# Kernel optimization log

Hardware: AMD Instinct MI355X
Metric: run time of the kernel (lower is better)

## Reference

```python
import jax, jax.numpy as jnp
import numpy as np
import math

HIDDEN = 1024
N_HEADS = 16
HEAD_DIM = HIDDEN // N_HEADS

def _safe(x, clamp_val):
    x = jnp.nan_to_num(x, nan=0.0, posinf=0.0, neginf=0.0)
    return jnp.clip(x, -clamp_val, clamp_val)

def _stable_linear(x, W, b):
    # StableLinear: clamp(50) -> linear -> clamp(50)
    x = _safe(x, 50.0)
    out = x @ W.T + b
    return _safe(out, 50.0)

def setup_inputs() -> dict:
    key = jax.random.key(0)
    ks = jax.random.split(key, 12)
    bsz, q_len, kv_len = 4, 1024, 2048
    q = jax.random.normal(ks[0], (bsz, q_len, HIDDEN), dtype=jnp.float32)
    kv = jax.random.normal(ks[1], (bsz, kv_len, HIDDEN), dtype=jnp.float32)
    key_padding_mask = jax.random.bernoulli(ks[2], 0.1, (bsz, kv_len))
    bound = 1.0 / math.sqrt(HIDDEN)
    def mk_w(k):
        return jax.random.uniform(k, (HIDDEN, HIDDEN), jnp.float32, -bound, bound)
    def mk_b(k):
        return jax.random.uniform(k, (HIDDEN,), jnp.float32, -bound, bound)
    return {
        'q': q, 'kv': kv, 'key_padding_mask': key_padding_mask,
        'Wq': mk_w(ks[3]), 'bq': mk_b(ks[4]),
        'Wk': mk_w(ks[5]), 'bk': mk_b(ks[6]),
        'Wv': mk_w(ks[7]), 'bv': mk_b(ks[8]),
        'Wo': mk_w(ks[9]), 'bo': mk_b(ks[10]),
    }

def reference(q, kv, key_padding_mask, Wq, bq, Wk, bk, Wv, bv, Wo, bo):
    bsz, q_len, _ = q.shape
    kv_len = kv.shape[1]
    # outer _safe(50) then StableLinear's own _safe(50) (idempotent)
    qh = _stable_linear(_safe(q, 50.0), Wq, bq)
    kh = _stable_linear(_safe(kv, 50.0), Wk, bk)
    vh = _stable_linear(_safe(kv, 50.0), Wv, bv)
    # [b, h, s, d]
    qh = qh.reshape(bsz, q_len, N_HEADS, HEAD_DIM).transpose(0, 2, 1, 3)
    kh = kh.reshape(bsz, kv_len, N_HEADS, HEAD_DIM).transpose(0, 2, 1, 3)
    vh = vh.reshape(bsz, kv_len, N_HEADS, HEAD_DIM).transpose(0, 2, 1, 3)
    scores = jnp.einsum('bhqd,bhkd->bhqk', qh.astype(jnp.float32), kh.astype(jnp.float32))
    scores = scores / math.sqrt(HEAD_DIM)
    scores = jnp.clip(scores, -80.0, 80.0)
    scores = jnp.where(key_padding_mask[:, None, None, :], -10000.0, scores)
    attn = jax.nn.softmax(scores, axis=-1)  # dropout is identity in eval mode
    out = jnp.einsum('bhqk,bhkd->bhqd', attn, vh.astype(jnp.float32))
    out = out.transpose(0, 2, 1, 3).reshape(bsz, q_len, HIDDEN)
    out = _stable_linear(_safe(out, 50.0), Wo, bo)
    return _safe(out, 50.0)
```

## Files before the change

### kernel.cpp

```cpp
#include <hip/hip_runtime.h>
#include <hip/hip_bf16.h>
#include <stdint.h>
#include <math.h>

#define HIDDEN 1024
#define NHEADS 16
#define HDIM   64
#define BSZ    4
#define QLEN   1024
#define KVLEN  2048

typedef __bf16 bf16_t;
typedef __bf16 bf16x8 __attribute__((ext_vector_type(8)));
typedef __bf16 bf16x4 __attribute__((ext_vector_type(4)));
typedef float  f32x4  __attribute__((ext_vector_type(4)));

#define C_SCALE 0.18033688f
#define C_FMADD (-43.2808512f)

#define GLOAD16(g, l) \
    __builtin_amdgcn_global_load_lds((const __attribute__((address_space(1))) void*)(g), \
                                     (__attribute__((address_space(3))) void*)(l), 16, 0, 0)

__device__ __forceinline__ float clamp50(float v) {
    return fminf(fmaxf(v, -50.f), 50.f);
}

#define NQ4  ((BSZ * QLEN  * HIDDEN) / 4)
#define NKV4 ((BSZ * KVLEN * HIDDEN) / 4)
#define NW4  ((HIDDEN * HIDDEN) / 4)
#define NCVT ((NQ4 + NKV4 + 4 * NW4) / 256)

__global__ void cvt_all_kernel(const float* __restrict__ q, const float* __restrict__ kv,
                               const float* __restrict__ W0, const float* __restrict__ W1,
                               const float* __restrict__ W2, const float* __restrict__ W3,
                               bf16_t* __restrict__ q_bf, bf16_t* __restrict__ kv_bf,
                               bf16_t* __restrict__ w_bf,
                               const void* __restrict__ msk, float* __restrict__ maskadd) {
    if (blockIdx.x >= NCVT) {
        __shared__ int s_float, s_multi;
        const int t = threadIdx.x;
        if (t == 0) { s_float = 0; s_multi = 0; }
        __syncthreads();
        const uint32_t* w = (const uint32_t*)msk;
        int cf = 0, cm = 0;
        for (int i = t; i < 2048; i += 256) {
            uint32_t v = w[i];
            if (v == 0x3F800000u) cf++;
            else if (v & 0xFFFFFF00u) cm++;
        }
        if (cf) atomicAdd(&s_float, cf);
        if (cm) atomicAdd(&s_multi, cm);
        __syncthreads();
        const int mode = (s_float > 0) ? 2 : ((s_multi > 0) ? 0 : 1);
        const int base = (blockIdx.x - NCVT) * 2048;
        for (int i = base + t; i < base + 2048; i += 256) {
            bool m;
            if (mode == 2)      m = ((const float*)msk)[i] != 0.0f;
            else if (mode == 1) m = ((const int*)msk)[i] != 0;
            else                m = ((const unsigned char*)msk)[i] != 0;
            maskadd[i] = m ? (-100000.0f + C_FMADD) : C_FMADD;
        }
        return;
    }
    const int i = blockIdx.x * blockDim.x + threadIdx.x;
    const float4* src;
    bf16x4* dst;
    if (i < NQ4) {
        src = (const float4*)q + i;            dst = (bf16x4*)q_bf + i;
    } else if (i < NQ4 + NKV4) {
        const int j = i - NQ4;
        src = (const float4*)kv + j;           dst = (bf16x4*)kv_bf + j;
    } else {
        const int j = i - (NQ4 + NKV4);
        const int ws = j >> 18, off = j & (NW4 - 1);
        const float* W = (ws == 0) ? W0 : (ws == 1) ? W1 : (ws == 2) ? W2 : W3;
        src = (const float4*)W + off;          dst = (bf16x4*)w_bf + (size_t)ws * NW4 + off;
    }
    const float4 v = *src;
    bf16x4 o;
    o[0] = (bf16_t)clamp50(v.x); o[1] = (bf16_t)clamp50(v.y);
    o[2] = (bf16_t)clamp50(v.z); o[3] = (bf16_t)clamp50(v.w);
    *dst = o;
}

template <int NT>
__device__ __forceinline__ void gemm_core(const char* __restrict__ Ab, const char* __restrict__ Bb,
                                          bf16_t* Als, bf16_t* Bls,
                                          f32x4 (&acc)[4][NT / 32],
                                          int wave, int lane, int wm, int wn)
{
    constexpr int NF = NT / 32;
    const int srcsw = ((lane & 7) ^ (lane >> 3)) << 4;
    const int rowl = lane >> 3;

    for (int kt = 0; kt < HIDDEN / 64; ++kt) {
#pragma unroll
        for (int i = 0; i < 4; ++i) {
            const int row = i * 32 + wave * 8 + rowl;
            GLOAD16(Ab + (size_t)row * (HIDDEN * 2) + kt * 128 + srcsw,
                    (char*)Als + i * 4096 + wave * 1024);
        }
#pragma unroll
        for (int i = 0; i < NF; ++i) {
            const int row = i * 32 + wave * 8 + rowl;
            GLOAD16(Bb + (size_t)row * (HIDDEN * 2) + kt * 128 + srcsw,
                    (char*)Bls + i * 4096 + wave * 1024);
        }
        __syncthreads();
#pragma unroll
        for (int kc = 0; kc < 2; ++kc) {
            const int kbyte = kc * 64 + ((lane >> 4) << 4);
            bf16x8 af[4], bfr[NF];
#pragma unroll
            for (int f2 = 0; f2 < 4; ++f2) {
                const int arow = wm * 64 + f2 * 16 + (lane & 15);
                af[f2] = *(const bf16x8*)((const char*)Als + arow * 128 + (kbyte ^ ((arow & 7) << 4)));
            }
#pragma unroll
            for (int f2 = 0; f2 < NF; ++f2) {
                const int brow = wn * (NT / 2) + f2 * 16 + (lane & 15);
                bfr[f2] = *(const bf16x8*)((const char*)Bls + brow * 128 + (kbyte ^ ((brow & 7) << 4)));
            }
#pragma unroll
            for (int mf = 0; mf < 4; ++mf)
#pragma unroll
                for (int nf = 0; nf < NF; ++nf)
                    acc[mf][nf] = __builtin_amdgcn_mfma_f32_16x16x32_bf16(af[mf], bfr[nf], acc[mf][nf], 0, 0, 0);
        }
        __syncthreads();
    }
}

template <int NF>
__device__ __forceinline__ void epi_head(f32x4 (&acc)[4][NF], const float* bias,
                                         bf16_t* out, int m0, int n0, int slog,
                                         int wm, int wn, int lane)
{
#pragma unroll
    for (int mf = 0; mf < 4; ++mf) {
#pragma unroll
        for (int nf = 0; nf < NF; ++nf) {
            const int gn = n0 + wn * (NF * 16) + nf * 16 + (lane & 15);
            const float bv = bias[gn];
#pragma unroll
            for (int r = 0; r < 4; ++r) {
                const int gm = m0 + wm * 64 + mf * 16 + ((lane >> 4) << 2) + r;
                const float v = clamp50(acc[mf][nf][r] + bv);
                const int b = gm >> slog;
                const int s = gm & ((1 << slog) - 1);
                const int h = gn >> 6, d = gn & 63;
                out[((((size_t)(b * NHEADS + h)) << slog) + s) * HDIM + d] = (bf16_t)v;
            }
        }
    }
}

template <int EPI, int NT>
__global__ __launch_bounds__(256)
void gemm_bt_kernel(const bf16_t* __restrict__ A, const bf16_t* __restrict__ B,
                    const float* __restrict__ bias, void* __restrict__ out, int slog)
{
    constexpr int NF = NT / 32;
    __shared__ __align__(16) bf16_t Smem[(128 + NT) * 64];
    bf16_t* Als = Smem;
    bf16_t* Bls = Smem + 128 * 64;

    const int m0 = blockIdx.y * 128;
    const int n0 = blockIdx.x * NT;
    const int t = threadIdx.x;
    const int wave = t >> 6, lane = t & 63;
    const int wm = wave >> 1, wn = wave & 1;

    f32x4 acc[4][NF] = {};
    gemm_core<NT>((const char*)A + (size_t)m0 * (HIDDEN * 2),
                  (const char*)B + (size_t)n0 * (HIDDEN * 2),
                  Als, Bls, acc, wave, lane, wm, wn);

    if (EPI == 0) {
        epi_head<NF>(acc, bias, (bf16_t*)out, m0, n0, slog, wm, wn, lane);
    } else {
#pragma unroll
        for (int mf = 0; mf < 4; ++mf) {
#pragma unroll
            for (int nf = 0; nf < NF; ++nf) {
                const int gn = n0 + wn * (NF * 16) + nf * 16 + (lane & 15);
                const float bv = bias[gn];
#pragma unroll
                for (int r = 0; r < 4; ++r) {
                    const int gm = m0 + wm * 64 + mf * 16 + ((lane >> 4) << 2) + r;
                    ((float*)out)[(size_t)gm * HIDDEN + gn] = clamp50(acc[mf][nf][r] + bv);
                }
            }
        }
    }
}

__global__ __launch_bounds__(256)
void gemm_kv_fused(const bf16_t* __restrict__ A, const bf16_t* __restrict__ Bk,
                   const bf16_t* __restrict__ Bv, const float* __restrict__ bk,
                   const float* __restrict__ bv, bf16_t* __restrict__ kh,
                   bf16_t* __restrict__ vt)
{
    __shared__ __align__(16) bf16_t Smem[2 * 128 * 64];
    bf16_t* Als = Smem;
    bf16_t* Bls = Smem + 128 * 64;

    const int isV = blockIdx.x >> 3;
    const int n0 = (blockIdx.x & 7) * 128;
    const int m0 = blockIdx.y * 128;
    const int t = threadIdx.x;
    const int wave = t >> 6, lane = t & 63;
    const int wm = wave >> 1, wn = wave & 1;
    const bf16_t* B = isV ? Bv : Bk;
    const float* bias = isV ? bv : bk;

    f32x4 acc[4][4] = {};
    gemm_core<128>((const char*)A + (size_t)m0 * (HIDDEN * 2),
                   (const char*)B + (size_t)n0 * (HIDDEN * 2),
                   Als, Bls, acc, wave, lane, wm, wn);

    if (!isV) {
        epi_head<4>(acc, bias, kh, m0, n0, 11, wm, wn, lane);
        return;
    }

    bf16_t* Cls = Smem;
    const int dl = t >> 1;
    const int sh = (t & 1) << 5;
    const int gn = n0 + dl;
    const int h = gn >> 6, d = gn & 63;
    const int bb = m0 >> 11;
    bf16_t* dst = vt + ((size_t)((bb * NHEADS + h) * HDIM + d)) * KVLEN
                + (m0 & (KVLEN - 1)) + sh;
#pragma unroll
    for (int ph = 0; ph < 2; ++ph) {
        if (wm == ph) {
#pragma unroll
            for (int mf = 0; mf < 4; ++mf) {
#pragma unroll
                for (int nf = 0; nf < 4; ++nf) {
                    const int dcol = wn * 64 + nf * 16 + (lane & 15);
                    const float bv2 = bias[n0 + dcol];
#pragma unroll
                    for (int r = 0; r < 4; ++r) {
                        const int srow = mf * 16 + ((lane >> 4) << 2) + r;
                        Cls[srow * 130 + dcol] = (bf16_t)clamp50(acc[mf][nf][r] + bv2);
                    }
                }
            }
        }
        __syncthreads();
#pragma unroll
        for (int j0 = 0; j0 < 32; j0 += 8) {
            bf16x8 v;
#pragma unroll
            for (int j = 0; j < 8; ++j) v[j] = Cls[(sh + j0 + j) * 130 + dl];
            *(bf16x8*)(dst + ph * 64 + j0) = v;
        }
        __syncthreads();
    }
}

__global__ __launch_bounds__(512)
void attn_fwd_kernel(const bf16_t* __restrict__ Qh, const bf16_t* __restrict__ Kh,
                     const bf16_t* __restrict__ Vt, const float* __restrict__ maskadd,
                     bf16_t* __restrict__ aout)
{
    __shared__ __align__(16) bf16_t Kls[2][64 * 64];
    __shared__ __align__(16) bf16_t Vls[2][64 * 64];
    __shared__ __align__(16) float Cbuf[4][32 * 64];
    __shared__ float Lbuf[4][2][16];

    const int f = blockIdx.x;
    const int o = (f & 7) * 64 + (f >> 3);
    const int qt = o & 7;
    const int bh = o >> 3;
    const int b = bh >> 4, h = bh & 15;
    const int t = threadIdx.x, wave = t >> 6, lane = t & 63;
    const int wq = wave & 3;
    const int wg = wave >> 2;
    const int g = lane >> 4, ql = lane & 15;

    const int qbase = qt * 128 + wq * 32;
    bf16x8 qf[2][2];
#pragma unroll
    for (int qq = 0; qq < 2; ++qq) {
        const bf16_t* qp = Qh + ((size_t)bh * QLEN + qbase + qq * 16 + ql) * HDIM + (g << 3);
        qf[qq][0] = *(const bf16x8*)qp;
        qf[qq][1] = *(const bf16x8*)(qp + 32);
    }

    f32x4 oacc[2][4] = {};
    float lsum[2] = {0.f, 0.f};

    const int srcsw = ((lane & 7) ^ (lane >> 3)) << 4;
    const int R = wave * 8 + (lane >> 3);
    const int kap = 32 * (R >> 5) + 8 * ((R >> 2) & 3) + 4 * ((R >> 4) & 1) + (R & 3);

    const char* Kb = (const char*)(Kh + (size_t)bh * KVLEN * HDIM);
    const char* Vb = (const char*)(Vt + (size_t)bh * HDIM * KVLEN);
    const float* mrow = maskadd + b * KVLEN + wg * 32 + g * 8;
    const int kb0 = g << 4;
    const int vcol = wg * 64 + kb0;

    GLOAD16(Kb + (size_t)kap * 128 + srcsw, (char*)&Kls[0][0] + wave * 1024);
    GLOAD16(Vb + (size_t)R * (KVLEN * 2) + srcsw, (char*)&Vls[0][0] + wave * 1024);
    f32x4 madd_c[2], madd_n[2];
    madd_c[0] = *(const f32x4*)(mrow);
    madd_c[1] = *(const f32x4*)(mrow + 4);
    __syncthreads();

    for (int kt = 0; kt < KVLEN / 64; ++kt) {
        const int cur = kt & 1;
        if (kt < KVLEN / 64 - 1) {
            const size_t ko = (size_t)(kt + 1) * 8192;
            GLOAD16(Kb + ko + (size_t)kap * 128 + srcsw,
                    (char*)&Kls[cur ^ 1][0] + wave * 1024);
            GLOAD16(Vb + (size_t)R * (KVLEN * 2) + (size_t)(kt + 1) * 128 + srcsw,
                    (char*)&Vls[cur ^ 1][0] + wave * 1024);
            madd_n[0] = *(const f32x4*)(mrow + (kt + 1) * 64);
            madd_n[1] = *(const f32x4*)(mrow + (kt + 1) * 64 + 4);
        }
        const char* Kc = (const char*)&Kls[cur][0];
        const char* Vc = (const char*)&Vls[cur][0];

        f32x4 sacc[2][2] = {};
#pragma unroll
        for (int kb = 0; kb < 2; ++kb) {
            const int key = wg * 32 + kb * 16 + ql;
            const int rowoff = key * 128;
            const int sw = (key & 7) << 4;
            const bf16x8 kf0 = *(const bf16x8*)(Kc + rowoff + ((kb0)      ^ sw));
            const bf16x8 kf1 = *(const bf16x8*)(Kc + rowoff + ((kb0 + 64) ^ sw));
#pragma unroll
            for (int qq = 0; qq < 2; ++qq) {
                sacc[qq][kb] = __builtin_amdgcn_mfma_f32_16x16x32_bf16(kf0, qf[qq][0], sacc[qq][kb], 0, 0, 0);
                sacc[qq][kb] = __builtin_amdgcn_mfma_f32_16x16x32_bf16(kf1, qf[qq][1], sacc[qq][kb], 0, 0, 0);
            }
        }

        bf16x8 pa[2];
#pragma unroll
        for (int qq = 0; qq < 2; ++qq) {
            float pv[2][4];
            float ls = 0.f;
#pragma unroll
            for (int kb = 0; kb < 2; ++kb) {
#pragma unroll
                for (int r = 0; r < 4; ++r) {
                    pv[kb][r] = __builtin_amdgcn_exp2f(
                        __builtin_fmaf(sacc[qq][kb][r], C_SCALE, madd_c[kb][r]));
                    ls += pv[kb][r];
                }
            }
            lsum[qq] += ls;
#pragma unroll
            for (int r = 0; r < 4; ++r) {
                pa[qq][r]     = (bf16_t)pv[0][r];
                pa[qq][4 + r] = (bf16_t)pv[1][r];
            }
        }

#pragma unroll
        for (int db = 0; db < 4; ++db) {
            const int vrow = db * 16 + ql;
            const int vsw = (vrow & 7) << 4;
            const bf16x8 vf = *(const bf16x8*)(Vc + vrow * 128 + (vcol ^ vsw));
#pragma unroll
            for (int qq = 0; qq < 2; ++qq)
                oacc[qq][db] = __builtin_amdgcn_mfma_f32_16x16x32_bf16(pa[qq], vf, oacc[qq][db], 0, 0, 0);
        }

        __syncthreads();
#pragma unroll
        for (int kb = 0; kb < 2; ++kb) madd_c[kb] = madd_n[kb];
    }

#pragma unroll
    for (int qq = 0; qq < 2; ++qq) {
        float l = lsum[qq];
        l += __shfl_xor(l, 16);
        l += __shfl_xor(l, 32);
        lsum[qq] = l;
    }
    const int rbase = g << 2;
    if (wg == 1) {
#pragma unroll
        for (int qq = 0; qq < 2; ++qq) {
#pragma unroll
            for (int db = 0; db < 4; ++db)
#pragma unroll
                for (int r = 0; r < 4; ++r)
                    Cbuf[wq][(qq * 16 + rbase + r) * 64 + db * 16 + ql] = oacc[qq][db][r];
            if (lane < 16) Lbuf[wq][qq][lane] = lsum[qq];
        }
    }
    __syncthreads();
    if (wg == 0) {
#pragma unroll
        for (int qq = 0; qq < 2; ++qq) {
            const float Lq = lsum[qq] + Lbuf[wq][qq][ql];
#pragma unroll
            for (int r = 0; r < 4; ++r) {
                const float Lr = __shfl(Lq, rbase + r);
                const float inv = 1.0f / Lr;
                const int qrow = qbase + qq * 16 + rbase + r;
                bf16_t* orow = aout + ((size_t)(b * QLEN + qrow)) * HIDDEN + h * HDIM;
#pragma unroll
                for (int db = 0; db < 4; ++db) {
                    const float add = Cbuf[wq][(qq * 16 + rbase + r) * 64 + db * 16 + ql];
                    orow[db * 16 + ql] = (bf16_t)((oacc[qq][db][r] + add) * inv);
                }
            }
        }
    }
}

extern "C" void kernel_launch(void* const* d_in, const int* in_sizes, int n_in,
                              void* d_out, int out_size, void* d_ws, size_t ws_size,
                              hipStream_t stream) {
    (void)in_sizes; (void)n_in; (void)out_size; (void)ws_size;
    const float* q   = (const float*)d_in[0];
    const float* kv  = (const float*)d_in[1];
    const void*  msk = d_in[2];
    const float* Wq  = (const float*)d_in[3];
    const float* bq  = (const float*)d_in[4];
    const float* Wk  = (const float*)d_in[5];
    const float* bk  = (const float*)d_in[6];
    const float* Wv  = (const float*)d_in[7];
    const float* bv  = (const float*)d_in[8];
    const float* Wo  = (const float*)d_in[9];
    const float* bo  = (const float*)d_in[10];

    char* ws = (char*)d_ws;
    const size_t MB = 1024 * 1024;
    float*  maskadd = (float*)ws;
    bf16_t* w_bf  = (bf16_t*)(ws + 32 * 1024);
    bf16_t* q_bf  = (bf16_t*)(ws + 32 * 1024 + 8  * MB);
    bf16_t* kv_bf = (bf16_t*)(ws + 32 * 1024 + 16 * MB);
    bf16_t* qh    = (bf16_t*)(ws + 32 * 1024 + 32 * MB);
    bf16_t* kh    = (bf16_t*)(ws + 32 * 1024 + 40 * MB);
    bf16_t* vt    = (bf16_t*)(ws + 32 * 1024 + 56 * MB);
    bf16_t* aout  = q_bf;

    bf16_t* wq_bf = w_bf;
    bf16_t* wk_bf = w_bf + (size_t)HIDDEN * HIDDEN;
    bf16_t* wv_bf = w_bf + (size_t)2 * HIDDEN * HIDDEN;
    bf16_t* wo_bf = w_bf + (size_t)3 * HIDDEN * HIDDEN;

    cvt_all_kernel<<<dim3(NCVT + 4), 256, 0, stream>>>(
        q, kv, Wq, Wk, Wv, Wo, q_bf, kv_bf, w_bf, msk, maskadd);

    gemm_bt_kernel<0, 64><<<dim3(16, 32), 256, 0, stream>>>(q_bf, wq_bf, bq, qh, 10);
    gemm_kv_fused<<<dim3(16, 64), 256, 0, stream>>>(kv_bf, wk_bf, wv_bf, bk, bv, kh, vt);

    attn_fwd_kernel<<<dim3(512), 512, 0, stream>>>(qh, kh, vt, maskadd, aout);

    gemm_bt_kernel<1, 64><<<dim3(16, 32), 256, 0, stream>>>(aout, wo_bf, bo, d_out, 10);
}
```

Before: 155.7 us.

## Merge Q/K/V projections into one launch and raise MFMA priority in attention

Combines the Q projection GEMM and the fused K/V projection GEMM into a single 1280-block kernel. Each block is mapped to a Q, K or V tile through a remapped block id that spreads consecutive blocks across segments, which removes one launch and the tail gap between the two GEMMs. The Q projection now uses 128-wide N tiles instead of 64. The attention loop also wraps its MFMA sections in s_setprio(1)/s_setprio(0) so the matrix-core work gets scheduling priority over the exp sections. Larger Q tiles reduce the block count and may change occupancy and load balance.

Result: no change. 153.9 us (-1.2%).

```diff
diff --git a/kernel.cpp b/kernel.cpp
--- a/kernel.cpp
+++ b/kernel.cpp
@@ -156,71 +156,45 @@
     }
 }
 
-template <int EPI, int NT>
 __global__ __launch_bounds__(256)
-void gemm_bt_kernel(const bf16_t* __restrict__ A, const bf16_t* __restrict__ B,
-                    const float* __restrict__ bias, void* __restrict__ out, int slog)
-{
-    constexpr int NF = NT / 32;
-    __shared__ __align__(16) bf16_t Smem[(128 + NT) * 64];
-    bf16_t* Als = Smem;
-    bf16_t* Bls = Smem + 128 * 64;
-
-    const int m0 = blockIdx.y * 128;
-    const int n0 = blockIdx.x * NT;
-    const int t = threadIdx.x;
-    const int wave = t >> 6, lane = t & 63;
-    const int wm = wave >> 1, wn = wave & 1;
-
-    f32x4 acc[4][NF] = {};
-    gemm_core<NT>((const char*)A + (size_t)m0 * (HIDDEN * 2),
-                  (const char*)B + (size_t)n0 * (HIDDEN * 2),
-                  Als, Bls, acc, wave, lane, wm, wn);
-
-    if (EPI == 0) {
-        epi_head<NF>(acc, bias, (bf16_t*)out, m0, n0, slog, wm, wn, lane);
-    } else {
-#pragma unroll
-        for (int mf = 0; mf < 4; ++mf) {
-#pragma unroll
-            for (int nf = 0; nf < NF; ++nf) {
-                const int gn = n0 + wn * (NF * 16) + nf * 16 + (lane & 15);
-                const float bv = bias[gn];
-#pragma unroll
-                for (int r = 0; r < 4; ++r) {
-                    const int gm = m0 + wm * 64 + mf * 16 + ((lane >> 4) << 2) + r;
-                    ((float*)out)[(size_t)gm * HIDDEN + gn] = clamp50(acc[mf][nf][r] + bv);
-                }
-            }
-        }
-    }
-}
-
-__global__ __launch_bounds__(256)
-void gemm_kv_fused(const bf16_t* __restrict__ A, const bf16_t* __restrict__ Bk,
-                   const bf16_t* __restrict__ Bv, const float* __restrict__ bk,
-                   const float* __restrict__ bv, bf16_t* __restrict__ kh,
+void gemm_proj_all(const bf16_t* __restrict__ q_bf, const bf16_t* __restrict__ kv_bf,
+                   const bf16_t* __restrict__ w_bf,
+                   const float* __restrict__ bq, const float* __restrict__ bk,
+                   const float* __restrict__ bv,
+                   bf16_t* __restrict__ qh, bf16_t* __restrict__ kh,
                    bf16_t* __restrict__ vt)
 {
     __shared__ __align__(16) bf16_t Smem[2 * 128 * 64];
     bf16_t* Als = Smem;
     bf16_t* Bls = Smem + 128 * 64;
 
-    const int isV = blockIdx.x >> 3;
-    const int n0 = (blockIdx.x & 7) * 128;
-    const int m0 = blockIdx.y * 128;
+    const int bid = blockIdx.x;
+    const int lid = (bid & 7) * 160 + (bid >> 3);
+
+    int seg, j;
+    if (lid < 256)      { seg = 0; j = lid; }
+    else if (lid < 768) { seg = 1; j = lid - 256; }
+    else                { seg = 2; j = lid - 768; }
+    const int m0 = (j >> 3) * 128;
+    const int n0 = (j & 7) * 128;
+    const bf16_t* A    = (seg == 0) ? q_bf : kv_bf;
+    const bf16_t* B    = w_bf + (size_t)seg * (HIDDEN * HIDDEN);
+    const float*  bias = (seg == 0) ? bq : (seg == 1) ? bk : bv;
+
     const int t = threadIdx.x;
     const int wave = t >> 6, lane = t & 63;
     const int wm = wave >> 1, wn = wave & 1;
-    const bf16_t* B = isV ? Bv : Bk;
-    const float* bias = isV ? bv : bk;
 
     f32x4 acc[4][4] = {};
     gemm_core<128>((const char*)A + (size_t)m0 * (HIDDEN * 2),
                    (const char*)B + (size_t)n0 * (HIDDEN * 2),
                    Als, Bls, acc, wave, lane, wm, wn);
 
-    if (!isV) {
+    if (seg == 0) {
+        epi_head<4>(acc, bias, qh, m0, n0, 10, wm, wn, lane);
+        return;
+    }
+    if (seg == 1) {
         epi_head<4>(acc, bias, kh, m0, n0, 11, wm, wn, lane);
         return;
     }
@@ -255,10 +229,46 @@
         for (int j0 = 0; j0 < 32; j0 += 8) {
             bf16x8 v;
 #pragma unroll
-            for (int j = 0; j < 8; ++j) v[j] = Cls[(sh + j0 + j) * 130 + dl];
+            for (int jj = 0; jj < 8; ++jj) v[jj] = Cls[(sh + j0 + jj) * 130 + dl];
             *(bf16x8*)(dst + ph * 64 + j0) = v;
         }
         __syncthreads();
+    }
+}
+
+template <int NT>
+__global__ __launch_bounds__(256)
+void gemm_out_kernel(const bf16_t* __restrict__ A, const bf16_t* __restrict__ B,
+                     const float* __restrict__ bias, float* __restrict__ out)
+{
+    constexpr int NF = NT / 32;
+    __shared__ __align__(16) bf16_t Smem[(128 + NT) * 64];
+    bf16_t* Als = Smem;
+    bf16_t* Bls = Smem + 128 * 64;
+
+    const int m0 = blockIdx.y * 128;
+    const int n0 = blockIdx.x * NT;
+    const int t = threadIdx.x;
+    const int wave = t >> 6, lane = t & 63;
+    const int wm = wave >> 1, wn = wave & 1;
+
+    f32x4 acc[4][NF] = {};
+    gemm_core<NT>((const char*)A + (size_t)m0 * (HIDDEN * 2),
+                  (const char*)B + (size_t)n0 * (HIDDEN * 2),
+                  Als, Bls, acc, wave, lane, wm, wn);
+
+#pragma unroll
+    for (int mf = 0; mf < 4; ++mf) {
+#pragma unroll
+        for (int nf = 0; nf < NF; ++nf) {
+            const int gn = n0 + wn * (NF * 16) + nf * 16 + (lane & 15);
+            const float bv = bias[gn];
+#pragma unroll
+            for (int r = 0; r < 4; ++r) {
+                const int gm = m0 + wm * 64 + mf * 16 + ((lane >> 4) << 2) + r;
+                out[(size_t)gm * HIDDEN + gn] = clamp50(acc[mf][nf][r] + bv);
+            }
+        }
     }
 }
 
@@ -326,6 +336,7 @@
         const char* Vc = (const char*)&Vls[cur][0];
 
         f32x4 sacc[2][2] = {};
+        __builtin_amdgcn_s_setprio(1);
 #pragma unroll
         for (int kb = 0; kb < 2; ++kb) {
             const int key = wg * 32 + kb * 16 + ql;
@@ -339,6 +350,7 @@
                 sacc[qq][kb] = __builtin_amdgcn_mfma_f32_16x16x32_bf16(kf1, qf[qq][1], sacc[qq][kb], 0, 0, 0);
             }
         }
+        __builtin_amdgcn_s_setprio(0);
 
         bf16x8 pa[2];
 #pragma unroll
@@ -362,6 +374,7 @@
             }
         }
 
+        __builtin_amdgcn_s_setprio(1);
 #pragma unroll
         for (int db = 0; db < 4; ++db) {
             const int vrow = db * 16 + ql;
@@ -371,6 +384,7 @@
             for (int qq = 0; qq < 2; ++qq)
                 oacc[qq][db] = __builtin_amdgcn_mfma_f32_16x16x32_bf16(pa[qq], vf, oacc[qq][db], 0, 0, 0);
         }
+        __builtin_amdgcn_s_setprio(0);
 
         __syncthreads();
 #pragma unroll
@@ -444,18 +458,15 @@
     bf16_t* vt    = (bf16_t*)(ws + 32 * 1024 + 56 * MB);
     bf16_t* aout  = q_bf;
 
-    bf16_t* wq_bf = w_bf;
-    bf16_t* wk_bf = w_bf + (size_t)HIDDEN * HIDDEN;
-    bf16_t* wv_bf = w_bf + (size_t)2 * HIDDEN * HIDDEN;
     bf16_t* wo_bf = w_bf + (size_t)3 * HIDDEN * HIDDEN;
 
     cvt_all_kernel<<<dim3(NCVT + 4), 256, 0, stream>>>(
         q, kv, Wq, Wk, Wv, Wo, q_bf, kv_bf, w_bf, msk, maskadd);
 
-    gemm_bt_kernel<0, 64><<<dim3(16, 32), 256, 0, stream>>>(q_bf, wq_bf, bq, qh, 10);
-    gemm_kv_fused<<<dim3(16, 64), 256, 0, stream>>>(kv_bf, wk_bf, wv_bf, bk, bv, kh, vt);
+    gemm_proj_all<<<dim3(1280), 256, 0, stream>>>(
+        q_bf, kv_bf, w_bf, bq, bk, bv, qh, kh, vt);
 
     attn_fwd_kernel<<<dim3(512), 512, 0, stream>>>(qh, kh, vt, maskadd, aout);
 
-    gemm_bt_kernel<1, 64><<<dim3(16, 32), 256, 0, stream>>>(aout, wo_bf, bo, d_out, 10);
-}
+    gemm_out_kernel<64><<<dim3(16, 32), 256, 0, stream>>>(aout, wo_bf, bo, (float*)d_out);
+}
```
